# Kernel tuning notes

Measured on AMD Instinct MI355X. Metric: run time of the kernel, lower is better.

The kernel has to match this reference:

```python
import jax, jax.numpy as jnp
import numpy as np

N = 4096
IN_F = 512
OUT_F = 1024
HEADS = 8
HEAD_F = OUT_F // HEADS  # 128
NEG_SLOPE = 0.2


def setup_inputs() -> dict:
    key = jax.random.key(0)
    ks = jax.random.split(key, 7)
    x = jax.random.normal(ks[0], (N, IN_F), dtype=jnp.float32)
    graph = jax.random.randint(ks[1], (N, N), 0, 2, dtype=jnp.int32)
    # xavier-normal-ish init scales
    W = jax.random.normal(ks[2], (HEADS, IN_F, HEAD_F), dtype=jnp.float32) * (2.0 / (IN_F + HEAD_F)) ** 0.5
    w_i = jax.random.normal(ks[3], (HEADS, HEAD_F, 1), dtype=jnp.float32) * (2.0 / (HEAD_F + 1)) ** 0.5
    w_j = jax.random.normal(ks[4], (HEADS, HEAD_F, 1), dtype=jnp.float32) * (2.0 / (HEAD_F + 1)) ** 0.5
    W_r = jax.random.normal(ks[5], (IN_F, HEAD_F * HEADS), dtype=jnp.float32) * (2.0 / (IN_F + HEAD_F * HEADS)) ** 0.5
    bias = jnp.zeros((OUT_F,), dtype=jnp.float32)
    return {"x": x, "graph": graph, "W": W, "w_i": w_i, "w_j": w_j, "W_r": W_r, "bias": bias}


def reference(x, graph, W, w_i, w_j, W_r, bias):
    # h: [H, N, F] = x @ W per head
    h = jnp.einsum('nm,hmf->hnf', x, W)
    coe_i = jnp.einsum('hnf,hfo->hno', h, w_i)              # [H, N, 1]
    coe_j = jnp.einsum('hnf,hfo->hno', h, w_j).transpose(0, 2, 1)  # [H, 1, N]
    coe = jax.nn.leaky_relu(coe_i + coe_j, negative_slope=NEG_SLOPE)  # [H, N, N]
    # adjacency mask: note the transpose as in the original (graph.t())
    mask = jnp.where(graph.T > 0, 0.0, -jnp.inf).astype(h.dtype)  # [N, N]
    att = jax.nn.softmax(coe + mask[None], axis=-1)          # [H, N, N]
    y = jnp.einsum('hnm,hmf->nhf', att, h)                   # [N, H, F]
    # mapped residual (in_features != head_features)
    y = y + (x @ W_r).reshape(-1, HEADS, HEAD_F)
    # concat heads
    y = y.reshape(-1, OUT_F)
    return y + bias
```

## Files before the change

kernel.cpp:

```cpp
#include <hip/hip_runtime.h>
#include <hip/hip_fp16.h>

typedef _Float16 f16;
typedef _Float16 f16x8 __attribute__((ext_vector_type(8)));
typedef _Float16 f16x2v __attribute__((ext_vector_type(2)));
typedef __fp16 h16x2 __attribute__((ext_vector_type(2)));
typedef float f32x4 __attribute__((ext_vector_type(4)));
typedef float f32x16 __attribute__((ext_vector_type(16)));

#define LOG2E 1.4426950408889634f
#define NSL 0.2f

__global__ __launch_bounds__(256) void k_a(const float* __restrict__ x,
                                           f16* __restrict__ xh2,
                                           const float* __restrict__ W,
                                           f16* __restrict__ Wht2,
                                           const float* __restrict__ Wr,
                                           f16* __restrict__ Wrt2,
                                           unsigned int* __restrict__ M2e) {
    __shared__ float tile[32][33];
    int bx = blockIdx.x;
    int tid = threadIdx.x;
    if (bx == 0 && tid < 8) M2e[tid] = 0x007FFFFFu;
    if (bx < 512) {
        int id = bx * 256 + tid;
        int row = id & 4095, kt = id >> 12;
        const float4* xs = (const float4*)(x + (size_t)row * 512 + kt * 16);
        float4 u0 = xs[0], u1 = xs[1], u2 = xs[2], u3 = xs[3];
        union { int4 a[2]; h16x2 p[8]; } px;
        px.p[0] = __builtin_amdgcn_cvt_pkrtz(u0.x, u0.y);
        px.p[1] = __builtin_amdgcn_cvt_pkrtz(u0.z, u0.w);
        px.p[2] = __builtin_amdgcn_cvt_pkrtz(u1.x, u1.y);
        px.p[3] = __builtin_amdgcn_cvt_pkrtz(u1.z, u1.w);
        px.p[4] = __builtin_amdgcn_cvt_pkrtz(u2.x, u2.y);
        px.p[5] = __builtin_amdgcn_cvt_pkrtz(u2.z, u2.w);
        px.p[6] = __builtin_amdgcn_cvt_pkrtz(u3.x, u3.y);
        px.p[7] = __builtin_amdgcn_cvt_pkrtz(u3.z, u3.w);
        int4* d = (int4*)(xh2 + ((size_t)kt * 4096 + row) * 16);
        d[0] = px.a[0]; d[1] = px.a[1];
    } else {
        const float* in; f16* out; int C, S, bxx, byy;
        if (bx < 1024) { int id = bx - 512;  in = W;  out = Wht2; C = 128;  S = 128;  bxx = id & 3;  byy = id >> 2; }
        else           { int id = bx - 1024; in = Wr; out = Wrt2; C = 1024; S = 1024; bxx = id & 31; byy = id >> 5; }
        int tx = tid & 31, ty = tid >> 5;
        int c0 = bxx * 32, r0 = byy * 32;
        for (int rr = ty; rr < 32; rr += 8)
            tile[rr][tx] = in[(r0 + rr) * C + c0 + tx];
        __syncthreads();
        for (int rr = ty; rr < 32; rr += 8) {
            int m = r0 + tx, f = c0 + rr;
            out[(size_t)((m >> 4) * S + f) * 16 + (m & 15)] = (f16)tile[tx][rr];
        }
    }
}

__global__ __launch_bounds__(256, 4) void k_b(const f16* __restrict__ xh2,
                                              const f16* __restrict__ Wht2,
                                              f16* __restrict__ hbT2,
                                              const float* __restrict__ wi,
                                              const float* __restrict__ wj,
                                              float* __restrict__ a2,
                                              float* __restrict__ b2,
                                              unsigned int* __restrict__ M2e,
                                              const int* __restrict__ graph,
                                              unsigned int* __restrict__ maskJ) {
    __shared__ float swi[128], swj[128];
    __shared__ float pwa[4][32], pwb[4][32];
    int bx = blockIdx.x;
    int tid = threadIdx.x;
    int w = tid >> 6, lane = tid & 63;

    if (bx >= 1024) {
        int e = (bx - 1024) * 256 + tid;
        int jw = e >> 12, ii = e & 4095;
        const int* gp = graph + (size_t)(jw << 5) * 4096 + ii;
        int gv[32];
        #pragma unroll
        for (int k = 0; k < 32; k++) gv[k] = gp[(size_t)k * 4096];
        unsigned word = 0;
        #pragma unroll
        for (int k = 0; k < 32; k++) word |= (gv[k] > 0) ? (1u << k) : 0u;
        maskJ[e] = word;
        return;
    }

    int h = bx & 7, jb = bx >> 3;
    int j0 = jb * 32;
    int ln = lane & 15, q = lane >> 4;
    if (tid < 128) { swi[tid] = wi[h * 128 + tid]; swj[tid] = wj[h * 128 + tid]; }
    __syncthreads();

    int ko = (q & 1) * 8;
    const f16* pa = Wht2 + ((size_t)(h * 512) * 8 + (size_t)(q >> 1) * 128 + w * 32 + ln) * 16 + ko;
    const f16* pb = xh2 + ((size_t)(q >> 1) * 4096 + j0 + ln) * 16 + ko;

    f32x4 acc00 = {}, acc01 = {}, acc10 = {}, acc11 = {};

    f16x8 ra0 = *(const f16x8*)(pa);
    f16x8 ra1 = *(const f16x8*)(pa + 256);
    f16x8 rb0 = *(const f16x8*)(pb);
    f16x8 rb1 = *(const f16x8*)(pb + 256);

    for (int kk = 0; kk < 8; kk++) {
        f16x8 sa0 = *(const f16x8*)(pa + 4096);
        f16x8 sa1 = *(const f16x8*)(pa + 4096 + 256);
        f16x8 sb0 = *(const f16x8*)(pb + 131072);
        f16x8 sb1 = *(const f16x8*)(pb + 131072 + 256);
        acc00 = __builtin_amdgcn_mfma_f32_16x16x32_f16(ra0, rb0, acc00, 0, 0, 0);
        acc01 = __builtin_amdgcn_mfma_f32_16x16x32_f16(ra0, rb1, acc01, 0, 0, 0);
        acc10 = __builtin_amdgcn_mfma_f32_16x16x32_f16(ra1, rb0, acc10, 0, 0, 0);
        acc11 = __builtin_amdgcn_mfma_f32_16x16x32_f16(ra1, rb1, acc11, 0, 0, 0);
        pa += 8192; pb += 262144;
        ra0 = *(const f16x8*)(pa);
        ra1 = *(const f16x8*)(pa + 256);
        rb0 = *(const f16x8*)(pb);
        rb1 = *(const f16x8*)(pb + 256);
        acc00 = __builtin_amdgcn_mfma_f32_16x16x32_f16(sa0, sb0, acc00, 0, 0, 0);
        acc01 = __builtin_amdgcn_mfma_f32_16x16x32_f16(sa0, sb1, acc01, 0, 0, 0);
        acc10 = __builtin_amdgcn_mfma_f32_16x16x32_f16(sa1, sb0, acc10, 0, 0, 0);
        acc11 = __builtin_amdgcn_mfma_f32_16x16x32_f16(sa1, sb1, acc11, 0, 0, 0);
    }

    size_t hb = (size_t)h * 524288 + (size_t)(j0 >> 4) * 2048;
    #pragma unroll
    for (int r = 0; r < 4; r++) {
        int f0 = w * 32 + q * 4 + r;
        hbT2[hb + f0 * 16 + ln]                 = (f16)acc00[r];
        hbT2[hb + 2048 + f0 * 16 + ln]          = (f16)acc01[r];
        hbT2[hb + (f0 + 16) * 16 + ln]          = (f16)acc10[r];
        hbT2[hb + 2048 + (f0 + 16) * 16 + ln]   = (f16)acc11[r];
    }

    float pa0 = 0.f, pb0 = 0.f, pa1 = 0.f, pb1 = 0.f;
    #pragma unroll
    for (int r = 0; r < 4; r++) {
        int f0 = w * 32 + q * 4 + r;
        float w0 = swi[f0], jv0 = swj[f0];
        float w1 = swi[f0 + 16], jv1 = swj[f0 + 16];
        pa0 += acc00[r] * w0 + acc10[r] * w1;
        pb0 += acc00[r] * jv0 + acc10[r] * jv1;
        pa1 += acc01[r] * w0 + acc11[r] * w1;
        pb1 += acc01[r] * jv0 + acc11[r] * jv1;
    }
    pa0 += __shfl_xor(pa0, 16); pa0 += __shfl_xor(pa0, 32);
    pb0 += __shfl_xor(pb0, 16); pb0 += __shfl_xor(pb0, 32);
    pa1 += __shfl_xor(pa1, 16); pa1 += __shfl_xor(pa1, 32);
    pb1 += __shfl_xor(pb1, 16); pb1 += __shfl_xor(pb1, 32);
    if (lane < 16) {
        pwa[w][ln] = pa0;      pwb[w][ln] = pb0;
        pwa[w][16 + ln] = pa1; pwb[w][16 + ln] = pb1;
    }
    __syncthreads();
    if (tid < 32) {
        int jj = tid;
        float pav = (pwa[0][jj] + pwa[1][jj]) + (pwa[2][jj] + pwa[3][jj]);
        float pbv = (pwb[0][jj] + pwb[1][jj]) + (pwb[2][jj] + pwb[3][jj]);
        a2[h * 4096 + j0 + jj] = pav * LOG2E;
        float bb = pbv * LOG2E;
        b2[h * 4096 + j0 + jj] = bb;
        float m = bb;
        m = fmaxf(m, __shfl_xor(m, 1, 32));
        m = fmaxf(m, __shfl_xor(m, 2, 32));
        m = fmaxf(m, __shfl_xor(m, 4, 32));
        m = fmaxf(m, __shfl_xor(m, 8, 32));
        m = fmaxf(m, __shfl_xor(m, 16, 32));
        if (jj == 0) {
            unsigned u = __float_as_uint(m);
            unsigned enc = (u & 0x80000000u) ? ~u : (u | 0x80000000u);
            atomicMax(&M2e[h], enc);
        }
    }
}

#define PGEN2(af, m8, qv, qw, A1, A2, DS)                                            \
    {                                                                                \
        union { int4 i4; unsigned u[4]; } uv, uw;                                    \
        uv.i4 = (qv); uw.i4 = (qw);                                                  \
        f16x2v dl = {(_Float16)0, (_Float16)0};                                      \
        _Pragma("unroll")                                                            \
        for (int p = 0; p < 4; p++) {                                                \
            union { unsigned u; f16x2v v; } b1, b2x, mm;                             \
            b1.u = uv.u[p]; b2x.u = uw.u[p];                                         \
            f16x2v pr1 = (A1) * b1.v;                                                \
            f16x2v pr2 = (A2) * b2x.v;                                               \
            mm.v = __builtin_elementwise_max(pr1, pr2);                              \
            int mlo = -(int)(((m8) >> (2 * p)) & 1u);                                \
            int mhi = -(int)(((m8) >> (2 * p + 1)) & 1u);                            \
            unsigned comb = ((unsigned)mlo & 0xFFFFu) | ((unsigned)mhi & 0xFFFF0000u);\
            mm.u &= comb;                                                            \
            af.u[p] = mm.u;                                                          \
            dl += mm.v;                                                              \
        }                                                                            \
        DS += (float)dl.x + (float)dl.y;                                             \
    }

#define PUTACC(dp, off, accv)                                                    \
    {                                                                            \
        union { f32x16 v; f32x4 q[4]; } t; t.v = (accv);                         \
        *(f32x4*)((dp) + (off))      = t.q[0];                                   \
        *(f32x4*)((dp) + (off) + 4)  = t.q[1];                                   \
        *(f32x4*)((dp) + (off) + 8)  = t.q[2];                                   \
        *(f32x4*)((dp) + (off) + 12) = t.q[3];                                   \
    }

#define ADDACC(dp, off, accv)                                                    \
    {                                                                            \
        union { f32x16 v; f32x4 q[4]; } t; t.v = (accv);                         \
        t.q[0] += *(const f32x4*)((dp) + (off));                                 \
        t.q[1] += *(const f32x4*)((dp) + (off) + 4);                             \
        t.q[2] += *(const f32x4*)((dp) + (off) + 8);                             \
        t.q[3] += *(const f32x4*)((dp) + (off) + 12);                            \
        (accv) = t.v;                                                            \
    }

__global__ __launch_bounds__(256, 2) void k_main(const f16* __restrict__ xh2,
                                                 const f16* __restrict__ hbT2,
                                                 const f16* __restrict__ Wrt2,
                                                 const unsigned int* __restrict__ maskJ,
                                                 const float* __restrict__ a2,
                                                 const float* __restrict__ b2,
                                                 const unsigned int* __restrict__ M2e,
                                                 const float* __restrict__ bias,
                                                 float* __restrict__ out) {
    __shared__ char smem[49664];
    __shared__ float dred[256];

    unsigned int* mlds = (unsigned int*)smem;
    unsigned int* bvlds = (unsigned int*)(smem + 33024);
    unsigned int* bwlds = (unsigned int*)(smem + 41216);

    int bx = blockIdx.x;
    int h = bx & 7, it = bx >> 3;
    int i0 = it * 64;
    int tid = threadIdx.x;
    int w = tid >> 6, lane = tid & 63;
    int l31 = lane & 31, half = lane >> 5;
    int i = i0 + l31;

    unsigned enc = M2e[h];
    unsigned um = (enc & 0x80000000u) ? (enc & 0x7FFFFFFFu) : ~enc;
    float M2 = __uint_as_float(um);

    {
        const float2* bsrc = (const float2*)(b2 + h * 4096);
        #pragma unroll
        for (int c = 0; c < 8; c++) {
            int p = tid + c * 256;
            float2 tb = bsrc[p];
            float t0 = tb.x - M2, t1 = tb.y - M2;
            union { h16x2 pp; unsigned ii; } k1, k2;
            k1.pp = __builtin_amdgcn_cvt_pkrtz(exp2f(t0), exp2f(t1));
            k2.pp = __builtin_amdgcn_cvt_pkrtz(exp2f(NSL * t0), exp2f(NSL * t1));
            bvlds[p] = k1.ii;
            bwlds[p] = k2.ii;
        }
        #pragma unroll
        for (int c = 0; c < 32; c++) {
            int e = tid + c * 256;
            int jw = e >> 6, ii = e & 63;
            mlds[ii * 129 + jw] = maskJ[(size_t)jw * 4096 + i0 + ii];
        }
    }

    float avL = a2[h * 4096 + i];
    float avH = a2[h * 4096 + i + 32];
    float uuL = avL + M2, uuH = avH + M2;
    float mvL = fmaxf(uuL, NSL * uuL);
    float mvH = fmaxf(uuH, NSL * uuH);
    union { h16x2 pp; f16x2v v; } apL, apH;
    apL.pp = __builtin_amdgcn_cvt_pkrtz(exp2f(uuL - mvL), exp2f(NSL * uuL - mvL));
    apH.pp = __builtin_amdgcn_cvt_pkrtz(exp2f(uuH - mvH), exp2f(NSL * uuH - mvH));
    f16x2v ApL1 = {apL.v.x, apL.v.x};
    f16x2v ApL2 = {apL.v.y, apL.v.y};
    f16x2v ApH1 = {apH.v.x, apH.v.x};
    f16x2v ApH2 = {apH.v.y, apH.v.y};

    f32x16 accL0 = {}, accL1 = {}, accL2 = {}, accL3 = {};
    f32x16 accH0 = {}, accH1 = {}, accH2 = {}, accH3 = {};
    float dsumL = 0.f, dsumH = 0.f;

    int J0 = w * 1024;
    const f16* bb = hbT2 + (size_t)h * 524288 + ((size_t)(J0 >> 4) * 128 + l31) * 16 + half * 8;
    const unsigned int* bpv = bvlds + (J0 >> 1) + half * 4;
    const unsigned int* bpw = bwlds + (J0 >> 1) + half * 4;
    const unsigned int* mrowL = mlds + l31 * 129 + (J0 >> 5);
    const unsigned int* mrowH = mlds + (l31 + 32) * 129 + (J0 >> 5);

    int sh0 = half << 3;
    int sh1 = 16 + (half << 3);

    __syncthreads();

    f16x8 fa0 = *(const f16x8*)(bb);
    f16x8 fa1 = *(const f16x8*)(bb + 512);
    f16x8 fa2 = *(const f16x8*)(bb + 1024);
    f16x8 fa3 = *(const f16x8*)(bb + 1536);
    int4 qv0 = ((const int4*)(bpv))[0];
    int4 qw0 = ((const int4*)(bpw))[0];
    unsigned mwcL = mrowL[0];
    unsigned mwcH = mrowH[0];

    for (int tp = 0; tp < 32; tp++) {
        int t0 = tp * 2;
        const f16* s1 = bb + (size_t)(t0 + 1) * 2048;
        f16x8 fb0 = *(const f16x8*)(s1);
        f16x8 fb1 = *(const f16x8*)(s1 + 512);
        f16x8 fb2 = *(const f16x8*)(s1 + 1024);
        f16x8 fb3 = *(const f16x8*)(s1 + 1536);
        int4 qv1 = *(const int4*)(bpv + (t0 + 1) * 8);
        int4 qw1 = *(const int4*)(bpw + (t0 + 1) * 8);
        unsigned mwnL = mrowL[tp + 1];
        unsigned mwnH = mrowH[tp + 1];

        {
            union { f16x8 v; unsigned u[4]; } af;
            PGEN2(af, mwcL >> sh0, qv0, qw0, ApL1, ApL2, dsumL);
            accL0 = __builtin_amdgcn_mfma_f32_32x32x16_f16(af.v, fa0, accL0, 0, 0, 0);
            accL1 = __builtin_amdgcn_mfma_f32_32x32x16_f16(af.v, fa1, accL1, 0, 0, 0);
            accL2 = __builtin_amdgcn_mfma_f32_32x32x16_f16(af.v, fa2, accL2, 0, 0, 0);
            accL3 = __builtin_amdgcn_mfma_f32_32x32x16_f16(af.v, fa3, accL3, 0, 0, 0);
        }
        {
            union { f16x8 v; unsigned u[4]; } af;
            PGEN2(af, mwcH >> sh0, qv0, qw0, ApH1, ApH2, dsumH);
            accH0 = __builtin_amdgcn_mfma_f32_32x32x16_f16(af.v, fa0, accH0, 0, 0, 0);
            accH1 = __builtin_amdgcn_mfma_f32_32x32x16_f16(af.v, fa1, accH1, 0, 0, 0);
            accH2 = __builtin_amdgcn_mfma_f32_32x32x16_f16(af.v, fa2, accH2, 0, 0, 0);
            accH3 = __builtin_amdgcn_mfma_f32_32x32x16_f16(af.v, fa3, accH3, 0, 0, 0);
        }

        const f16* s2 = bb + (size_t)(t0 + 2) * 2048;
        fa0 = *(const f16x8*)(s2);
        fa1 = *(const f16x8*)(s2 + 512);
        fa2 = *(const f16x8*)(s2 + 1024);
        fa3 = *(const f16x8*)(s2 + 1536);
        qv0 = *(const int4*)(bpv + (t0 + 2) * 8);
        qw0 = *(const int4*)(bpw + (t0 + 2) * 8);

        {
            union { f16x8 v; unsigned u[4]; } af;
            PGEN2(af, mwcL >> sh1, qv1, qw1, ApL1, ApL2, dsumL);
            accL0 = __builtin_amdgcn_mfma_f32_32x32x16_f16(af.v, fb0, accL0, 0, 0, 0);
            accL1 = __builtin_amdgcn_mfma_f32_32x32x16_f16(af.v, fb1, accL1, 0, 0, 0);
            accL2 = __builtin_amdgcn_mfma_f32_32x32x16_f16(af.v, fb2, accL2, 0, 0, 0);
            accL3 = __builtin_amdgcn_mfma_f32_32x32x16_f16(af.v, fb3, accL3, 0, 0, 0);
        }
        {
            union { f16x8 v; unsigned u[4]; } af;
            PGEN2(af, mwcH >> sh1, qv1, qw1, ApH1, ApH2, dsumH);
            accH0 = __builtin_amdgcn_mfma_f32_32x32x16_f16(af.v, fb0, accH0, 0, 0, 0);
            accH1 = __builtin_amdgcn_mfma_f32_32x32x16_f16(af.v, fb1, accH1, 0, 0, 0);
            accH2 = __builtin_amdgcn_mfma_f32_32x32x16_f16(af.v, fb2, accH2, 0, 0, 0);
            accH3 = __builtin_amdgcn_mfma_f32_32x32x16_f16(af.v, fb3, accH3, 0, 0, 0);
        }
        mwcL = mwnL;
        mwcH = mwnH;
    }

    dsumL += __shfl(dsumL, lane ^ 32);
    dsumH += __shfl(dsumH, lane ^ 32);
    if (lane < 32) {
        dred[w * 64 + l31] = dsumL;
        dred[w * 64 + 32 + l31] = dsumH;
    }
    __syncthreads();
    {
        #pragma unroll
        for (int r = 0; r < 16; r++) {
            int row = (r & 3) + 8 * (r >> 2) + 4 * half;
            float sL = dred[row] + dred[64 + row] + dred[128 + row] + dred[192 + row];
            float sH = dred[32 + row] + dred[96 + row] + dred[160 + row] + dred[224 + row];
            float invL = 1.0f / sL;
            float invH = 1.0f / sH;
            accL0[r] *= invL; accL1[r] *= invL; accL2[r] *= invL; accL3[r] *= invL;
            accH0[r] *= invH; accH1[r] *= invH; accH2[r] *= invH; accH3[r] *= invH;
        }
    }

    {
        #pragma unroll
        for (int kt = 0; kt < 8; kt++) {
            int ktt = w * 8 + kt;
            f16x8 axL = *(const f16x8*)(xh2 + ((size_t)ktt * 4096 + i) * 16 + half * 8);
            f16x8 axH = *(const f16x8*)(xh2 + ((size_t)ktt * 4096 + i + 32) * 16 + half * 8);
            const f16* wb = Wrt2 + ((size_t)ktt * 1024 + h * 128 + l31) * 16 + half * 8;
            f16x8 wb0 = *(const f16x8*)(wb);
            f16x8 wb1 = *(const f16x8*)(wb + 512);
            f16x8 wb2 = *(const f16x8*)(wb + 1024);
            f16x8 wb3 = *(const f16x8*)(wb + 1536);
            accL0 = __builtin_amdgcn_mfma_f32_32x32x16_f16(axL, wb0, accL0, 0, 0, 0);
            accL1 = __builtin_amdgcn_mfma_f32_32x32x16_f16(axL, wb1, accL1, 0, 0, 0);
            accL2 = __builtin_amdgcn_mfma_f32_32x32x16_f16(axL, wb2, accL2, 0, 0, 0);
            accL3 = __builtin_amdgcn_mfma_f32_32x32x16_f16(axL, wb3, accL3, 0, 0, 0);
            accH0 = __builtin_amdgcn_mfma_f32_32x32x16_f16(axH, wb0, accH0, 0, 0, 0);
            accH1 = __builtin_amdgcn_mfma_f32_32x32x16_f16(axH, wb1, accH1, 0, 0, 0);
            accH2 = __builtin_amdgcn_mfma_f32_32x32x16_f16(axH, wb2, accH2, 0, 0, 0);
            accH3 = __builtin_amdgcn_mfma_f32_32x32x16_f16(axH, wb3, accH3, 0, 0, 0);
        }
    }

    float* xredb = (float*)smem;

    __syncthreads();
    if (w >= 2) {
        float* dp = xredb + (w - 2) * 4352 + lane * 68;
        PUTACC(dp, 0, accL0); PUTACC(dp, 16, accL1); PUTACC(dp, 32, accL2); PUTACC(dp, 48, accL3);
    }
    __syncthreads();
    if (w < 2) {
        const float* dp = xredb + w * 4352 + lane * 68;
        ADDACC(dp, 0, accL0); ADDACC(dp, 16, accL1); ADDACC(dp, 32, accL2); ADDACC(dp, 48, accL3);
    }
    __syncthreads();
    if (w == 1) {
        float* dp = xredb + lane * 68;
        PUTACC(dp, 0, accL0); PUTACC(dp, 16, accL1); PUTACC(dp, 32, accL2); PUTACC(dp, 48, accL3);
    }
    __syncthreads();
    if (w == 0) {
        const float* dp = xredb + lane * 68;
        ADDACC(dp, 0, accL0); ADDACC(dp, 16, accL1); ADDACC(dp, 32, accL2); ADDACC(dp, 48, accL3);
        #pragma unroll
        for (int n = 0; n < 4; n++) {
            union { f32x16 v; f32x4 q[4]; } t;
            t.v = (n == 0) ? accL0 : (n == 1) ? accL1 : (n == 2) ? accL2 : accL3;
            int col = h * 128 + n * 32 + l31;
            float bv = bias[col];
            #pragma unroll
            for (int r = 0; r < 16; r++) {
                int row = i0 + (r & 3) + 8 * (r >> 2) + 4 * half;
                out[(size_t)row * 1024 + col] = t.v[r] + bv;
            }
        }
    }

    __syncthreads();
    if (w >= 2) {
        float* dp = xredb + (w - 2) * 4352 + lane * 68;
        PUTACC(dp, 0, accH0); PUTACC(dp, 16, accH1); PUTACC(dp, 32, accH2); PUTACC(dp, 48, accH3);
    }
    __syncthreads();
    if (w < 2) {
        const float* dp = xredb + w * 4352 + lane * 68;
        ADDACC(dp, 0, accH0); ADDACC(dp, 16, accH1); ADDACC(dp, 32, accH2); ADDACC(dp, 48, accH3);
    }
    __syncthreads();
    if (w == 1) {
        float* dp = xredb + lane * 68;
        PUTACC(dp, 0, accH0); PUTACC(dp, 16, accH1); PUTACC(dp, 32, accH2); PUTACC(dp, 48, accH3);
    }
    __syncthreads();
    if (w == 0) {
        const float* dp = xredb + lane * 68;
        ADDACC(dp, 0, accH0); ADDACC(dp, 16, accH1); ADDACC(dp, 32, accH2); ADDACC(dp, 48, accH3);
        #pragma unroll
        for (int n = 0; n < 4; n++) {
            union { f32x16 v; f32x4 q[4]; } t;
            t.v = (n == 0) ? accH0 : (n == 1) ? accH1 : (n == 2) ? accH2 : accH3;
            int col = h * 128 + n * 32 + l31;
            float bv = bias[col];
            #pragma unroll
            for (int r = 0; r < 16; r++) {
                int row = i0 + 32 + (r & 3) + 8 * (r >> 2) + 4 * half;
                out[(size_t)row * 1024 + col] = t.v[r] + bv;
            }
        }
    }
}

extern "C" void kernel_launch(void* const* d_in, const int* in_sizes, int n_in,
                              void* d_out, int out_size, void* d_ws, size_t ws_size,
                              hipStream_t stream) {
    (void)in_sizes; (void)n_in; (void)out_size; (void)ws_size;
    const float* x     = (const float*)d_in[0];
    const int*   graph = (const int*)d_in[1];
    const float* W     = (const float*)d_in[2];
    const float* wi    = (const float*)d_in[3];
    const float* wj    = (const float*)d_in[4];
    const float* Wr    = (const float*)d_in[5];
    const float* bias  = (const float*)d_in[6];
    float* out = (float*)d_out;

    char* ws = (char*)d_ws;
    unsigned int* maskJ = (unsigned int*)ws;
    f16* hbT2  = (f16*)(ws + (2u << 20));
    f16* Wht2  = (f16*)(ws + (10u << 20));
    f16* Wrt2  = (f16*)(ws + (11u << 20));
    f16* xh2   = (f16*)(ws + (12u << 20));
    float* a2    = (float*)(ws + (16u << 20));
    float* b2    = a2 + 8 * 4096;
    unsigned int* M2e = (unsigned int*)(b2 + 8 * 4096);

    hipLaunchKernelGGL(k_a, dim3(1536), dim3(256), 0, stream, x, xh2, W, Wht2, Wr, Wrt2, M2e);
    hipLaunchKernelGGL(k_b, dim3(3072), dim3(256), 0, stream, xh2, Wht2, hbT2,
                       wi, wj, a2, b2, M2e, graph, maskJ);
    hipLaunchKernelGGL(k_main, dim3(512), dim3(256), 0, stream, xh2, hbT2, Wrt2, maskJ,
                       a2, b2, M2e, bias, out);
}
```

Baseline: 183.1 us.

## Stream B tiles and mask via global_load_lds triple-buffered pipeline in main loop

```diff
diff --git a/kernel.cpp b/kernel.cpp
--- a/kernel.cpp
+++ b/kernel.cpp
@@ -10,6 +10,15 @@
 
 #define LOG2E 1.4426950408889634f
 #define NSL 0.2f
+
+__device__ __forceinline__ void gll16(const void* g, void* l) {
+    __builtin_amdgcn_global_load_lds((const __attribute__((address_space(1))) void*)g,
+                                     (__attribute__((address_space(3))) void*)l, 16, 0, 0);
+}
+__device__ __forceinline__ void gll4(const void* g, void* l) {
+    __builtin_amdgcn_global_load_lds((const __attribute__((address_space(1))) void*)g,
+                                     (__attribute__((address_space(3))) void*)l, 4, 0, 0);
+}
 
 __global__ __launch_bounds__(256) void k_a(const float* __restrict__ x,
                                            f16* __restrict__ xh2,
@@ -213,6 +222,63 @@
         (accv) = t.v;                                                            \
     }
 
+#define MMH(M8, QV, QW, A1, A2, DS, AC0, AC1, AC2, AC3, F0, F1, F2, F3)              \
+    {                                                                                \
+        union { f16x8 v; unsigned u[4]; } af;                                        \
+        PGEN2(af, M8, QV, QW, A1, A2, DS);                                           \
+        __builtin_amdgcn_s_setprio(1);                                               \
+        AC0 = __builtin_amdgcn_mfma_f32_32x32x16_f16(af.v, F0, AC0, 0, 0, 0);        \
+        AC1 = __builtin_amdgcn_mfma_f32_32x32x16_f16(af.v, F1, AC1, 0, 0, 0);        \
+        AC2 = __builtin_amdgcn_mfma_f32_32x32x16_f16(af.v, F2, AC2, 0, 0, 0);        \
+        AC3 = __builtin_amdgcn_mfma_f32_32x32x16_f16(af.v, F3, AC3, 0, 0, 0);        \
+        __builtin_amdgcn_s_setprio(0);                                               \
+    }
+
+#define TP(K, CA, CB, PA, PB, MR, MW)                                                \
+    {                                                                                \
+        int4 qv1 = *(const int4*)(bpv + (2 * (K) + 1) * 8);                          \
+        int4 qw1 = *(const int4*)(bpw + (2 * (K) + 1) * 8);                          \
+        __builtin_amdgcn_sched_barrier(0);                                           \
+        {                                                                            \
+            const char* g2 = bbB + (size_t)(2 * (K) + 2) * 4096;                     \
+            gll16(g2,        fwb + (PA) * 4096);                                     \
+            gll16(g2 + 1024, fwb + (PA) * 4096 + 1024);                              \
+            gll16(g2 + 2048, fwb + (PA) * 4096 + 2048);                              \
+            gll16(g2 + 3072, fwb + (PA) * 4096 + 3072);                              \
+            gll4(mgB + (size_t)((K) + 1) * 16384, mwb + (MW) * 256);                 \
+        }                                                                            \
+        asm volatile("s_waitcnt vmcnt(9)" ::: "memory");                             \
+        unsigned mwL = *(const unsigned*)(mrl + (MR) * 256);                         \
+        unsigned mwH = *(const unsigned*)(mrl + (MR) * 256 + 128);                   \
+        {                                                                            \
+            f16x8 f0 = *(const f16x8*)(lrp + (CA) * 4096);                           \
+            f16x8 f1 = *(const f16x8*)(lrp + (CA) * 4096 + 1024);                    \
+            f16x8 f2 = *(const f16x8*)(lrp + (CA) * 4096 + 2048);                    \
+            f16x8 f3 = *(const f16x8*)(lrp + (CA) * 4096 + 3072);                    \
+            MMH(mwL >> sh0, qv0, qw0, ApL1, ApL2, dsumL, accL0, accL1, accL2, accL3, f0, f1, f2, f3); \
+            MMH(mwH >> sh0, qv0, qw0, ApH1, ApH2, dsumH, accH0, accH1, accH2, accH3, f0, f1, f2, f3); \
+        }                                                                            \
+        qv0 = *(const int4*)(bpv + (2 * (K) + 2) * 8);                               \
+        qw0 = *(const int4*)(bpw + (2 * (K) + 2) * 8);                               \
+        __builtin_amdgcn_sched_barrier(0);                                           \
+        {                                                                            \
+            const char* g3 = bbB + (size_t)(2 * (K) + 3) * 4096;                     \
+            gll16(g3,        fwb + (PB) * 4096);                                     \
+            gll16(g3 + 1024, fwb + (PB) * 4096 + 1024);                              \
+            gll16(g3 + 2048, fwb + (PB) * 4096 + 2048);                              \
+            gll16(g3 + 3072, fwb + (PB) * 4096 + 3072);                              \
+        }                                                                            \
+        asm volatile("s_waitcnt vmcnt(9)" ::: "memory");                             \
+        {                                                                            \
+            f16x8 f0 = *(const f16x8*)(lrp + (CB) * 4096);                           \
+            f16x8 f1 = *(const f16x8*)(lrp + (CB) * 4096 + 1024);                    \
+            f16x8 f2 = *(const f16x8*)(lrp + (CB) * 4096 + 2048);                    \
+            f16x8 f3 = *(const f16x8*)(lrp + (CB) * 4096 + 3072);                    \
+            MMH(mwL >> sh1, qv1, qw1, ApL1, ApL2, dsumL, accL0, accL1, accL2, accL3, f0, f1, f2, f3); \
+            MMH(mwH >> sh1, qv1, qw1, ApH1, ApH2, dsumH, accH0, accH1, accH2, accH3, f0, f1, f2, f3); \
+        }                                                                            \
+    }
+
 __global__ __launch_bounds__(256, 2) void k_main(const f16* __restrict__ xh2,
                                                  const f16* __restrict__ hbT2,
                                                  const f16* __restrict__ Wrt2,
@@ -222,12 +288,11 @@
                                                  const unsigned int* __restrict__ M2e,
                                                  const float* __restrict__ bias,
                                                  float* __restrict__ out) {
-    __shared__ char smem[49664];
+    __shared__ char smem[68608];
     __shared__ float dred[256];
 
-    unsigned int* mlds = (unsigned int*)smem;
-    unsigned int* bvlds = (unsigned int*)(smem + 33024);
-    unsigned int* bwlds = (unsigned int*)(smem + 41216);
+    unsigned int* bvlds = (unsigned int*)(smem + 49152);
+    unsigned int* bwlds = (unsigned int*)(smem + 57344);
 
     int bx = blockIdx.x;
     int h = bx & 7, it = bx >> 3;
@@ -253,12 +318,6 @@
             k2.pp = __builtin_amdgcn_cvt_pkrtz(exp2f(NSL * t0), exp2f(NSL * t1));
             bvlds[p] = k1.ii;
             bwlds[p] = k2.ii;
-        }
-        #pragma unroll
-        for (int c = 0; c < 32; c++) {
-            int e = tid + c * 256;
-            int jw = e >> 6, ii = e & 63;
-            mlds[ii * 129 + jw] = maskJ[(size_t)jw * 4096 + i0 + ii];
         }
     }
 
@@ -283,79 +342,41 @@
     const f16* bb = hbT2 + (size_t)h * 524288 + ((size_t)(J0 >> 4) * 128 + l31) * 16 + half * 8;
     const unsigned int* bpv = bvlds + (J0 >> 1) + half * 4;
     const unsigned int* bpw = bwlds + (J0 >> 1) + half * 4;
-    const unsigned int* mrowL = mlds + l31 * 129 + (J0 >> 5);
-    const unsigned int* mrowH = mlds + (l31 + 32) * 129 + (J0 >> 5);
+
+    char* fwb = smem + w * 12288;
+    const char* lrp = fwb + lane * 16;
+    char* mwb = smem + 65536 + w * 768;
+    const char* mrl = mwb + l31 * 4;
+    const char* bbB = (const char*)bb;
+    const char* mgB = (const char*)(maskJ + (size_t)(J0 >> 5) * 4096 + i0) + lane * 4;
 
     int sh0 = half << 3;
     int sh1 = 16 + (half << 3);
 
     __syncthreads();
 
-    f16x8 fa0 = *(const f16x8*)(bb);
-    f16x8 fa1 = *(const f16x8*)(bb + 512);
-    f16x8 fa2 = *(const f16x8*)(bb + 1024);
-    f16x8 fa3 = *(const f16x8*)(bb + 1536);
+    gll4(mgB, mwb);
+    gll16(bbB,        fwb);
+    gll16(bbB + 1024, fwb + 1024);
+    gll16(bbB + 2048, fwb + 2048);
+    gll16(bbB + 3072, fwb + 3072);
+    gll16(bbB + 4096, fwb + 4096);
+    gll16(bbB + 5120, fwb + 4096 + 1024);
+    gll16(bbB + 6144, fwb + 4096 + 2048);
+    gll16(bbB + 7168, fwb + 4096 + 3072);
     int4 qv0 = ((const int4*)(bpv))[0];
     int4 qw0 = ((const int4*)(bpw))[0];
-    unsigned mwcL = mrowL[0];
-    unsigned mwcH = mrowH[0];
-
-    for (int tp = 0; tp < 32; tp++) {
-        int t0 = tp * 2;
-        const f16* s1 = bb + (size_t)(t0 + 1) * 2048;
-        f16x8 fb0 = *(const f16x8*)(s1);
-        f16x8 fb1 = *(const f16x8*)(s1 + 512);
-        f16x8 fb2 = *(const f16x8*)(s1 + 1024);
-        f16x8 fb3 = *(const f16x8*)(s1 + 1536);
-        int4 qv1 = *(const int4*)(bpv + (t0 + 1) * 8);
-        int4 qw1 = *(const int4*)(bpw + (t0 + 1) * 8);
-        unsigned mwnL = mrowL[tp + 1];
-        unsigned mwnH = mrowH[tp + 1];
-
-        {
-            union { f16x8 v; unsigned u[4]; } af;
-            PGEN2(af, mwcL >> sh0, qv0, qw0, ApL1, ApL2, dsumL);
-            accL0 = __builtin_amdgcn_mfma_f32_32x32x16_f16(af.v, fa0, accL0, 0, 0, 0);
-            accL1 = __builtin_amdgcn_mfma_f32_32x32x16_f16(af.v, fa1, accL1, 0, 0, 0);
-            accL2 = __builtin_amdgcn_mfma_f32_32x32x16_f16(af.v, fa2, accL2, 0, 0, 0);
-            accL3 = __builtin_amdgcn_mfma_f32_32x32x16_f16(af.v, fa3, accL3, 0, 0, 0);
-        }
-        {
-            union { f16x8 v; unsigned u[4]; } af;
-            PGEN2(af, mwcH >> sh0, qv0, qw0, ApH1, ApH2, dsumH);
-            accH0 = __builtin_amdgcn_mfma_f32_32x32x16_f16(af.v, fa0, accH0, 0, 0, 0);
-            accH1 = __builtin_amdgcn_mfma_f32_32x32x16_f16(af.v, fa1, accH1, 0, 0, 0);
-            accH2 = __builtin_amdgcn_mfma_f32_32x32x16_f16(af.v, fa2, accH2, 0, 0, 0);
-            accH3 = __builtin_amdgcn_mfma_f32_32x32x16_f16(af.v, fa3, accH3, 0, 0, 0);
-        }
-
-        const f16* s2 = bb + (size_t)(t0 + 2) * 2048;
-        fa0 = *(const f16x8*)(s2);
-        fa1 = *(const f16x8*)(s2 + 512);
-        fa2 = *(const f16x8*)(s2 + 1024);
-        fa3 = *(const f16x8*)(s2 + 1536);
-        qv0 = *(const int4*)(bpv + (t0 + 2) * 8);
-        qw0 = *(const int4*)(bpw + (t0 + 2) * 8);
-
-        {
-            union { f16x8 v; unsigned u[4]; } af;
-            PGEN2(af, mwcL >> sh1, qv1, qw1, ApL1, ApL2, dsumL);
-            accL0 = __builtin_amdgcn_mfma_f32_32x32x16_f16(af.v, fb0, accL0, 0, 0, 0);
-            accL1 = __builtin_amdgcn_mfma_f32_32x32x16_f16(af.v, fb1, accL1, 0, 0, 0);
-            accL2 = __builtin_amdgcn_mfma_f32_32x32x16_f16(af.v, fb2, accL2, 0, 0, 0);
-            accL3 = __builtin_amdgcn_mfma_f32_32x32x16_f16(af.v, fb3, accL3, 0, 0, 0);
-        }
-        {
-            union { f16x8 v; unsigned u[4]; } af;
-            PGEN2(af, mwcH >> sh1, qv1, qw1, ApH1, ApH2, dsumH);
-            accH0 = __builtin_amdgcn_mfma_f32_32x32x16_f16(af.v, fb0, accH0, 0, 0, 0);
-            accH1 = __builtin_amdgcn_mfma_f32_32x32x16_f16(af.v, fb1, accH1, 0, 0, 0);
-            accH2 = __builtin_amdgcn_mfma_f32_32x32x16_f16(af.v, fb2, accH2, 0, 0, 0);
-            accH3 = __builtin_amdgcn_mfma_f32_32x32x16_f16(af.v, fb3, accH3, 0, 0, 0);
-        }
-        mwcL = mwnL;
-        mwcH = mwnH;
-    }
+
+    #pragma unroll 1
+    for (int kk = 0; kk < 30; kk += 3) {
+        TP(kk,     0, 1, 2, 0, 0, 1)
+        TP(kk + 1, 2, 0, 1, 2, 1, 2)
+        TP(kk + 2, 1, 2, 0, 1, 2, 0)
+    }
+    TP(30, 0, 1, 2, 0, 0, 1)
+    TP(31, 2, 0, 1, 2, 1, 2)
+
+    asm volatile("s_waitcnt vmcnt(0)" ::: "memory");
 
     dsumL += __shfl(dsumL, lane ^ 32);
     dsumH += __shfl(dsumH, lane ^ 32);
```

New measurement: 191.4 us. +4.5%, slower.
